# Performance work log

Measured on AMD Instinct MI355X. Metric: run time of the kernel, lower is better.

## Reference

```python
import jax, jax.numpy as jnp
import numpy as np

B, V, H_DIM, W_DIM = 4, 4, 256, 384
D_SH = 1  # sh_degree=0, pred_color=False -> (0+1)^2
SCALE_MIN, SCALE_MAX = 1e-05, 30.0
EPS = 1e-08


def _quat_to_mat(q):  # (...,4) wxyz unit quat -> (...,3,3)
    w, x, y, z = q[..., 0], q[..., 1], q[..., 2], q[..., 3]
    return jnp.stack([
        jnp.stack([1 - 2 * (y * y + z * z), 2 * (x * y - w * z), 2 * (x * z + w * y)], -1),
        jnp.stack([2 * (x * y + w * z), 1 - 2 * (x * x + z * z), 2 * (y * z - w * x)], -1),
        jnp.stack([2 * (x * z - w * y), 2 * (y * z + w * x), 1 - 2 * (x * x + y * y)], -1),
    ], -2)


def _mat_to_quat_wxyz(m):  # (...,3,3) rotation -> (...,4) wxyz
    m00, m01, m02 = m[..., 0, 0], m[..., 0, 1], m[..., 0, 2]
    m10, m11, m12 = m[..., 1, 0], m[..., 1, 1], m[..., 1, 2]
    m20, m21, m22 = m[..., 2, 0], m[..., 2, 1], m[..., 2, 2]
    q_abs = jnp.sqrt(jnp.maximum(0.0, jnp.stack([
        1.0 + m00 + m11 + m22, 1.0 + m00 - m11 - m22,
        1.0 - m00 + m11 - m22, 1.0 - m00 - m11 + m22], -1)))
    cand = jnp.stack([
        jnp.stack([q_abs[..., 0] ** 2, m21 - m12, m02 - m20, m10 - m01], -1),
        jnp.stack([m21 - m12, q_abs[..., 1] ** 2, m10 + m01, m02 + m20], -1),
        jnp.stack([m02 - m20, m10 + m01, q_abs[..., 2] ** 2, m12 + m21], -1),
        jnp.stack([m10 - m01, m20 + m02, m21 + m12, q_abs[..., 3] ** 2], -1),
    ], -2)
    cand = cand / (2.0 * jnp.maximum(q_abs[..., None], 0.1))
    idx = jnp.argmax(q_abs, axis=-1)
    q = jnp.take_along_axis(cand, idx[..., None, None], axis=-2)[..., 0, :]
    return q / jnp.linalg.norm(q, axis=-1, keepdims=True)


def _quat_mul_wxyz(a, b):
    aw, ax, ay, az = a[..., 0], a[..., 1], a[..., 2], a[..., 3]
    bw, bx, by, bz = b[..., 0], b[..., 1], b[..., 2], b[..., 3]
    return jnp.stack([
        aw * bw - ax * bx - ay * by - az * bz,
        aw * bx + ax * bw + ay * bz - az * by,
        aw * by - ax * bz + ay * bw + az * bx,
        aw * bz + ax * by - ay * bx + az * bw], -1)


def setup_inputs() -> dict:
    key = jax.random.key(0)
    k1, k2, k3, k4, k5, k6 = jax.random.split(key, 6)
    # valid world->cam extrinsics: rotation from random unit quats + translation
    q = jax.random.normal(k1, (B, V, 4), jnp.float32)
    q = q / jnp.linalg.norm(q, axis=-1, keepdims=True)
    R = _quat_to_mat(q)
    t = jax.random.normal(k2, (B, V, 3), jnp.float32)
    ext = jnp.zeros((B, V, 4, 4), jnp.float32)
    ext = ext.at[..., :3, :3].set(R).at[..., :3, 3].set(t).at[..., 3, 3].set(1.0)
    # pixel-unit intrinsics
    f = W_DIM * (0.8 + 0.4 * jax.random.uniform(k3, (B, V), jnp.float32))
    intr = jnp.zeros((B, V, 3, 3), jnp.float32)
    intr = (intr.at[..., 0, 0].set(f).at[..., 1, 1].set(f)
                .at[..., 0, 2].set(W_DIM / 2).at[..., 1, 2].set(H_DIM / 2)
                .at[..., 2, 2].set(1.0))
    depths = 0.5 + 9.5 * jax.random.uniform(k4, (B, V, H_DIM, W_DIM), jnp.float32)
    opac = jax.random.uniform(k5, (B, V, H_DIM, W_DIM), jnp.float32)
    raw = jax.random.normal(k6, (B, V, H_DIM, W_DIM, 12), jnp.float32)
    return {"extrinsics": ext, "intrinsics": intr, "depths": depths,
            "opacities": opac, "raw_gaussians": raw, "H": H_DIM, "W": W_DIM}


def reference(extrinsics, intrinsics, depths, opacities, raw_gaussians, H, W):
    raw = raw_gaussians
    b, v = raw.shape[:2]
    dtype = raw.dtype
    # cam2world = affine inverse of world2cam extrinsics
    Rw2c = extrinsics[..., :3, :3]
    t = extrinsics[..., :3, 3]
    Rc2w = jnp.swapaxes(Rw2c, -1, -2)                       # (b,v,3,3)
    origins = -jnp.einsum('bvij,bvj->bvi', Rc2w, t)          # (b,v,3) camera centers
    # normalized intrinsics (detached in the original)
    intr_n = jax.lax.stop_gradient(intrinsics) * jnp.array(
        [[1.0 / W], [1.0 / H], [1.0]], dtype=intrinsics.dtype)
    # pixel-center grid in normalized [0,1] coords, (x, y) order
    xs = (jnp.arange(W, dtype=dtype) + 0.5) / W
    ys = (jnp.arange(H, dtype=dtype) + 0.5) / H
    xy = jnp.stack(jnp.meshgrid(xs, ys, indexing='xy'), -1)  # (H,W,2)
    pixel_size = jnp.array([1.0 / W, 1.0 / H], dtype=dtype)
    xy = xy[None, None] + raw[..., :2] * pixel_size          # (b,v,H,W,2) with xy offset
    # unproject: K^-1 @ [x,y,1], normalize, rotate into world
    Kinv = jnp.linalg.inv(intr_n)                            # (b,v,3,3)
    homog = jnp.concatenate([xy, jnp.ones_like(xy[..., :1])], -1)
    d_cam = jnp.einsum('bvij,bvhwj->bvhwi', Kinv, homog)
    d_cam = d_cam / jnp.linalg.norm(d_cam, axis=-1, keepdims=True)
    d_world = jnp.einsum('bvij,bvhwj->bvhwi', Rc2w, d_cam)
    means = origins[:, :, None, None] + d_world * depths[..., None]
    means = means.reshape(b, -1, 3)
    # scales: sigmoid squash then metric scaling by depth * intrinsics multiplier
    scales = SCALE_MIN + (SCALE_MAX - SCALE_MIN) * jax.nn.sigmoid(raw[..., 2:5])
    k2 = intr_n[..., :2, :2]
    det = k2[..., 0, 0] * k2[..., 1, 1] - k2[..., 0, 1] * k2[..., 1, 0]
    inv2 = jnp.stack([
        jnp.stack([k2[..., 1, 1], -k2[..., 0, 1]], -1),
        jnp.stack([-k2[..., 1, 0], k2[..., 0, 0]], -1)], -2) / det[..., None, None]
    mult = 0.1 * jnp.einsum('bvij,j->bvi', inv2, pixel_size).sum(-1)  # (b,v)
    gs_scales = (scales * depths[..., None] * mult[:, :, None, None, None]).reshape(b, -1, 3)
    # rotations: normalize predicted cam quat (xyzw), compose with c2w rotation -> world wxyz
    rot = raw[..., 5:9]
    rot = rot / (jnp.linalg.norm(rot, axis=-1, keepdims=True) + EPS)
    cam_q_wxyz = jnp.concatenate([rot[..., 3:4], rot[..., :3]], -1)
    c2w_q = _mat_to_quat_wxyz(Rc2w)                          # (b,v,4)
    world_q = _quat_mul_wxyz(c2w_q[:, :, None, None, :], cam_q_wxyz)
    rotations = world_q.reshape(b, -1, 4)
    # spherical harmonics: degree 0 -> sh_mask is all ones, no SH rotation
    harmonics = raw[..., 9:12].reshape(b, -1, 3, D_SH)
    opac = opacities.reshape(b, -1)
    return means, gs_scales, rotations, harmonics, opac
```

## Files before the change

kernel.cpp:

```cpp
#include <hip/hip_runtime.h>
#include <math.h>

#define Bc 4
#define Vc 4
#define Hc 256
#define Wc 384
#define HWc (Hc*Wc)
#define TOTc (Bc*Vc*HWc)
#define SCALE_MIN_c 1e-05f
#define SCALE_MAX_c 30.0f
#define EPS_c 1e-08f

#define MEANS_OFF  ((size_t)0)
#define SCALES_OFF ((size_t)TOTc*3)
#define ROT_OFF    ((size_t)TOTc*6)
#define HARM_OFF   ((size_t)TOTc*10)
#define OPAC_OFF   ((size_t)TOTc*13)

__device__ __forceinline__ void async_copy16(const float4* g, float4* l) {
    __builtin_amdgcn_global_load_lds(
        (const __attribute__((address_space(1))) void*)g,
        (__attribute__((address_space(3))) void*)l,
        16, 0, 0);
}

__global__ __launch_bounds__(256) void ga_kernel(
    const float* __restrict__ ext,
    const float* __restrict__ intr,
    const float* __restrict__ depths,
    const float* __restrict__ opac,
    const float* __restrict__ raw,
    float* __restrict__ out)
{
    __shared__ float4 sRaw[768];
    __shared__ float sR[9];
    __shared__ float sO[3];
    __shared__ float sK[9];
    __shared__ float sQ[4];
    __shared__ float sMult;
    __shared__ float sOut[2304];

    const int tid = threadIdx.x;
    const int g   = blockIdx.x * 256 + tid;

    {
        const float4* gbase = reinterpret_cast<const float4*>(raw) + (size_t)blockIdx.x * 768;
        const int waveBase = tid & 192;
        async_copy16(gbase +   0 + tid, &sRaw[  0 + waveBase]);
        async_copy16(gbase + 256 + tid, &sRaw[256 + waveBase]);
        async_copy16(gbase + 512 + tid, &sRaw[512 + waveBase]);
    }

    const float dep = depths[g];
    const float op  = opac[g];

    if (tid == 0) {
        const int view = blockIdx.x / (HWc / 256);
        const float* E = ext + view * 16;
        float R[9];
        #pragma unroll
        for (int i = 0; i < 3; i++)
            #pragma unroll
            for (int j = 0; j < 3; j++)
                R[i*3+j] = E[j*4+i];
        const float t0 = E[3], t1 = E[7], t2 = E[11];
        sO[0] = -(R[0]*t0 + R[1]*t1 + R[2]*t2);
        sO[1] = -(R[3]*t0 + R[4]*t1 + R[5]*t2);
        sO[2] = -(R[6]*t0 + R[7]*t1 + R[8]*t2);
        #pragma unroll
        for (int k = 0; k < 9; k++) sR[k] = R[k];

        const float* I = intr + view * 9;
        const float a00 = I[0]*(1.0f/Wc), a01 = I[1]*(1.0f/Wc), a02 = I[2]*(1.0f/Wc);
        const float a10 = I[3]*(1.0f/Hc), a11 = I[4]*(1.0f/Hc), a12 = I[5]*(1.0f/Hc);
        const float a20 = I[6],           a21 = I[7],           a22 = I[8];
        const float det = a00*(a11*a22 - a12*a21)
                        - a01*(a10*a22 - a12*a20)
                        + a02*(a10*a21 - a11*a20);
        const float id = 1.0f / det;
        sK[0] = (a11*a22 - a12*a21)*id;
        sK[1] = (a02*a21 - a01*a22)*id;
        sK[2] = (a01*a12 - a02*a11)*id;
        sK[3] = (a12*a20 - a10*a22)*id;
        sK[4] = (a00*a22 - a02*a20)*id;
        sK[5] = (a02*a10 - a00*a12)*id;
        sK[6] = (a10*a21 - a11*a20)*id;
        sK[7] = (a01*a20 - a00*a21)*id;
        sK[8] = (a00*a11 - a01*a10)*id;

        const float det2 = a00*a11 - a01*a10;
        const float psx = 1.0f/Wc, psy = 1.0f/Hc;
        sMult = 0.1f * ((a11*psx - a01*psy) + (-a10*psx + a00*psy)) / det2;

        const float m00 = R[0], m01 = R[1], m02 = R[2];
        const float m10 = R[3], m11 = R[4], m12 = R[5];
        const float m20 = R[6], m21 = R[7], m22 = R[8];
        float qa[4];
        qa[0] = sqrtf(fmaxf(0.0f, 1.0f + m00 + m11 + m22));
        qa[1] = sqrtf(fmaxf(0.0f, 1.0f + m00 - m11 - m22));
        qa[2] = sqrtf(fmaxf(0.0f, 1.0f - m00 + m11 - m22));
        qa[3] = sqrtf(fmaxf(0.0f, 1.0f - m00 - m11 + m22));
        float cand[4][4] = {
            { qa[0]*qa[0], m21 - m12,   m02 - m20,   m10 - m01 },
            { m21 - m12,   qa[1]*qa[1], m10 + m01,   m02 + m20 },
            { m02 - m20,   m10 + m01,   qa[2]*qa[2], m12 + m21 },
            { m10 - m01,   m20 + m02,   m21 + m12,   qa[3]*qa[3] } };
        int idx = 0;
        if (qa[1] > qa[idx]) idx = 1;
        if (qa[2] > qa[idx]) idx = 2;
        if (qa[3] > qa[idx]) idx = 3;
        const float dd = 1.0f / (2.0f * fmaxf(qa[idx], 0.1f));
        float q0 = cand[idx][0]*dd, q1 = cand[idx][1]*dd,
              q2 = cand[idx][2]*dd, q3 = cand[idx][3]*dd;
        const float qn = 1.0f / sqrtf(q0*q0 + q1*q1 + q2*q2 + q3*q3);
        sQ[0] = q0*qn; sQ[1] = q1*qn; sQ[2] = q2*qn; sQ[3] = q3*qn;
    }
    __syncthreads();

    const float4 r0 = sRaw[tid*3 + 0];
    const float4 r1 = sRaw[tid*3 + 1];
    const float4 r2 = sRaw[tid*3 + 2];

    const int pix = g % HWc;
    const int h = pix / Wc;
    const int w = pix % Wc;

    const float x = (w + 0.5f) * (1.0f/Wc) + r0.x * (1.0f/Wc);
    const float y = (h + 0.5f) * (1.0f/Hc) + r0.y * (1.0f/Hc);

    float dc0 = sK[0]*x + sK[1]*y + sK[2];
    float dc1 = sK[3]*x + sK[4]*y + sK[5];
    float dc2 = sK[6]*x + sK[7]*y + sK[8];
    const float inl = rsqrtf(dc0*dc0 + dc1*dc1 + dc2*dc2);
    dc0 *= inl; dc1 *= inl; dc2 *= inl;

    const float dw0 = sR[0]*dc0 + sR[1]*dc1 + sR[2]*dc2;
    const float dw1 = sR[3]*dc0 + sR[4]*dc1 + sR[5]*dc2;
    const float dw2 = sR[6]*dc0 + sR[7]*dc1 + sR[8]*dc2;

    sOut[tid*3 + 0] = sO[0] + dw0 * dep;
    sOut[tid*3 + 1] = sO[1] + dw1 * dep;
    sOut[tid*3 + 2] = sO[2] + dw2 * dep;

    const float sm = dep * sMult;
    sOut[768 + tid*3 + 0] = (SCALE_MIN_c + (SCALE_MAX_c - SCALE_MIN_c) / (1.0f + __expf(-r0.z))) * sm;
    sOut[768 + tid*3 + 1] = (SCALE_MIN_c + (SCALE_MAX_c - SCALE_MIN_c) / (1.0f + __expf(-r0.w))) * sm;
    sOut[768 + tid*3 + 2] = (SCALE_MIN_c + (SCALE_MAX_c - SCALE_MIN_c) / (1.0f + __expf(-r1.x))) * sm;

    const float rx = r1.y, ry = r1.z, rz = r1.w, rw = r2.x;
    const float rn = 1.0f / (sqrtf(rx*rx + ry*ry + rz*rz + rw*rw) + EPS_c);
    const float bw = rw*rn, bx = rx*rn, by = ry*rn, bz = rz*rn;
    const float aw = sQ[0], ax = sQ[1], ay = sQ[2], az = sQ[3];
    float4 wq;
    wq.x = aw*bw - ax*bx - ay*by - az*bz;
    wq.y = aw*bx + ax*bw + ay*bz - az*by;
    wq.z = aw*by - ax*bz + ay*bw + az*bx;
    wq.w = aw*bz + ax*by - ay*bx + az*bw;
    reinterpret_cast<float4*>(out + ROT_OFF)[g] = wq;

    sOut[1536 + tid*3 + 0] = r2.y;
    sOut[1536 + tid*3 + 1] = r2.z;
    sOut[1536 + tid*3 + 2] = r2.w;

    out[OPAC_OFF + g] = op;

    __syncthreads();

    const float4* sv = reinterpret_cast<const float4*>(sOut);
    #pragma unroll
    for (int i = tid; i < 576; i += 256) {
        const int sec = i / 192;
        const int j   = i - sec * 192;
        const size_t base = (sec == 0 ? MEANS_OFF : (sec == 1 ? SCALES_OFF : HARM_OFF))
                          + (size_t)blockIdx.x * 768;
        reinterpret_cast<float4*>(out + base)[j] = sv[i];
    }
}

extern "C" void kernel_launch(void* const* d_in, const int* in_sizes, int n_in,
                              void* d_out, int out_size, void* d_ws, size_t ws_size,
                              hipStream_t stream) {
    const float* ext    = (const float*)d_in[0];
    const float* intr   = (const float*)d_in[1];
    const float* depths = (const float*)d_in[2];
    const float* opac   = (const float*)d_in[3];
    const float* raw    = (const float*)d_in[4];
    float* out = (float*)d_out;

    ga_kernel<<<TOTc / 256, 256, 0, stream>>>(ext, intr, depths, opac, raw, out);
}
```

Measured before the change: 171.2 us.

## Compute per-view constants per thread and drop block barriers via per-wave LDS staging

Every thread now computes the per-view rotation, inverse intrinsics and camera quaternion redundantly instead of thread 0 writing them to shared memory. This removes the block-wide barrier and the separate output staging buffer. Each wave async-loads its own slice of raw data, waits with s_waitcnt, and reuses the same LDS slots to repack results. Output stores become per-lane scalar writes instead of float4 writes, and the launch bounds request higher occupancy. The trade is extra redundant ALU work and scalar loads per thread, plus narrower global stores, in exchange for fewer barriers and less LDS.

```diff
diff --git a/kernel.cpp b/kernel.cpp
--- a/kernel.cpp
+++ b/kernel.cpp
@@ -24,7 +24,7 @@
         16, 0, 0);
 }
 
-__global__ __launch_bounds__(256) void ga_kernel(
+__global__ __launch_bounds__(256, 6) void ga_kernel(
     const float* __restrict__ ext,
     const float* __restrict__ intr,
     const float* __restrict__ depths,
@@ -33,89 +33,92 @@
     float* __restrict__ out)
 {
     __shared__ float4 sRaw[768];
-    __shared__ float sR[9];
-    __shared__ float sO[3];
-    __shared__ float sK[9];
-    __shared__ float sQ[4];
-    __shared__ float sMult;
-    __shared__ float sOut[2304];
 
-    const int tid = threadIdx.x;
-    const int g   = blockIdx.x * 256 + tid;
+    const int tid  = threadIdx.x;
+    const int lane = tid & 63;
+    const int wv   = tid >> 6;
+    const int g    = blockIdx.x * 256 + tid;
 
     {
-        const float4* gbase = reinterpret_cast<const float4*>(raw) + (size_t)blockIdx.x * 768;
-        const int waveBase = tid & 192;
-        async_copy16(gbase +   0 + tid, &sRaw[  0 + waveBase]);
-        async_copy16(gbase + 256 + tid, &sRaw[256 + waveBase]);
-        async_copy16(gbase + 512 + tid, &sRaw[512 + waveBase]);
+        const float4* gbase = reinterpret_cast<const float4*>(raw)
+                            + (size_t)blockIdx.x * 768 + wv * 192;
+        float4* lbase = &sRaw[wv * 192];
+        async_copy16(gbase +   0 + lane, lbase +   0);
+        async_copy16(gbase +  64 + lane, lbase +  64);
+        async_copy16(gbase + 128 + lane, lbase + 128);
     }
 
     const float dep = depths[g];
     const float op  = opac[g];
 
-    if (tid == 0) {
-        const int view = blockIdx.x / (HWc / 256);
-        const float* E = ext + view * 16;
-        float R[9];
-        #pragma unroll
-        for (int i = 0; i < 3; i++)
-            #pragma unroll
-            for (int j = 0; j < 3; j++)
-                R[i*3+j] = E[j*4+i];
-        const float t0 = E[3], t1 = E[7], t2 = E[11];
-        sO[0] = -(R[0]*t0 + R[1]*t1 + R[2]*t2);
-        sO[1] = -(R[3]*t0 + R[4]*t1 + R[5]*t2);
-        sO[2] = -(R[6]*t0 + R[7]*t1 + R[8]*t2);
-        #pragma unroll
-        for (int k = 0; k < 9; k++) sR[k] = R[k];
+    const int view = blockIdx.x / (HWc / 256);
+    const float* E = ext  + view * 16;
+    const float* I = intr + view * 9;
 
-        const float* I = intr + view * 9;
-        const float a00 = I[0]*(1.0f/Wc), a01 = I[1]*(1.0f/Wc), a02 = I[2]*(1.0f/Wc);
-        const float a10 = I[3]*(1.0f/Hc), a11 = I[4]*(1.0f/Hc), a12 = I[5]*(1.0f/Hc);
-        const float a20 = I[6],           a21 = I[7],           a22 = I[8];
-        const float det = a00*(a11*a22 - a12*a21)
-                        - a01*(a10*a22 - a12*a20)
-                        + a02*(a10*a21 - a11*a20);
-        const float id = 1.0f / det;
-        sK[0] = (a11*a22 - a12*a21)*id;
-        sK[1] = (a02*a21 - a01*a22)*id;
-        sK[2] = (a01*a12 - a02*a11)*id;
-        sK[3] = (a12*a20 - a10*a22)*id;
-        sK[4] = (a00*a22 - a02*a20)*id;
-        sK[5] = (a02*a10 - a00*a12)*id;
-        sK[6] = (a10*a21 - a11*a20)*id;
-        sK[7] = (a01*a20 - a00*a21)*id;
-        sK[8] = (a00*a11 - a01*a10)*id;
+    const float R0 = E[0], R1 = E[4], R2 = E[8];
+    const float R3 = E[1], R4 = E[5], R5 = E[9];
+    const float R6 = E[2], R7 = E[6], R8 = E[10];
+    const float t0 = E[3], t1 = E[7], t2 = E[11];
+    const float O0 = -(R0*t0 + R1*t1 + R2*t2);
+    const float O1 = -(R3*t0 + R4*t1 + R5*t2);
+    const float O2 = -(R6*t0 + R7*t1 + R8*t2);
 
-        const float det2 = a00*a11 - a01*a10;
-        const float psx = 1.0f/Wc, psy = 1.0f/Hc;
-        sMult = 0.1f * ((a11*psx - a01*psy) + (-a10*psx + a00*psy)) / det2;
+    const float a00 = I[0]*(1.0f/Wc), a01 = I[1]*(1.0f/Wc), a02 = I[2]*(1.0f/Wc);
+    const float a10 = I[3]*(1.0f/Hc), a11 = I[4]*(1.0f/Hc), a12 = I[5]*(1.0f/Hc);
+    const float a20 = I[6],           a21 = I[7],           a22 = I[8];
+    const float det = a00*(a11*a22 - a12*a21)
+                    - a01*(a10*a22 - a12*a20)
+                    + a02*(a10*a21 - a11*a20);
+    const float id = 1.0f / det;
+    const float K0 = (a11*a22 - a12*a21)*id;
+    const float K1 = (a02*a21 - a01*a22)*id;
+    const float K2 = (a01*a12 - a02*a11)*id;
+    const float K3 = (a12*a20 - a10*a22)*id;
+    const float K4 = (a00*a22 - a02*a20)*id;
+    const float K5 = (a02*a10 - a00*a12)*id;
+    const float K6 = (a10*a21 - a11*a20)*id;
+    const float K7 = (a01*a20 - a00*a21)*id;
+    const float K8 = (a00*a11 - a01*a10)*id;
 
-        const float m00 = R[0], m01 = R[1], m02 = R[2];
-        const float m10 = R[3], m11 = R[4], m12 = R[5];
-        const float m20 = R[6], m21 = R[7], m22 = R[8];
-        float qa[4];
-        qa[0] = sqrtf(fmaxf(0.0f, 1.0f + m00 + m11 + m22));
-        qa[1] = sqrtf(fmaxf(0.0f, 1.0f + m00 - m11 - m22));
-        qa[2] = sqrtf(fmaxf(0.0f, 1.0f - m00 + m11 - m22));
-        qa[3] = sqrtf(fmaxf(0.0f, 1.0f - m00 - m11 + m22));
-        float cand[4][4] = {
-            { qa[0]*qa[0], m21 - m12,   m02 - m20,   m10 - m01 },
-            { m21 - m12,   qa[1]*qa[1], m10 + m01,   m02 + m20 },
-            { m02 - m20,   m10 + m01,   qa[2]*qa[2], m12 + m21 },
-            { m10 - m01,   m20 + m02,   m21 + m12,   qa[3]*qa[3] } };
-        int idx = 0;
-        if (qa[1] > qa[idx]) idx = 1;
-        if (qa[2] > qa[idx]) idx = 2;
-        if (qa[3] > qa[idx]) idx = 3;
-        const float dd = 1.0f / (2.0f * fmaxf(qa[idx], 0.1f));
-        float q0 = cand[idx][0]*dd, q1 = cand[idx][1]*dd,
-              q2 = cand[idx][2]*dd, q3 = cand[idx][3]*dd;
-        const float qn = 1.0f / sqrtf(q0*q0 + q1*q1 + q2*q2 + q3*q3);
-        sQ[0] = q0*qn; sQ[1] = q1*qn; sQ[2] = q2*qn; sQ[3] = q3*qn;
+    const float det2 = a00*a11 - a01*a10;
+    const float mult = 0.1f * ((a11*(1.0f/Wc) - a01*(1.0f/Hc))
+                             + (-a10*(1.0f/Wc) + a00*(1.0f/Hc))) / det2;
+
+    const float m00 = R0, m01 = R1, m02 = R2;
+    const float m10 = R3, m11 = R4, m12 = R5;
+    const float m20 = R6, m21 = R7, m22 = R8;
+    const float qa0 = sqrtf(fmaxf(0.0f, 1.0f + m00 + m11 + m22));
+    const float qa1 = sqrtf(fmaxf(0.0f, 1.0f + m00 - m11 - m22));
+    const float qa2 = sqrtf(fmaxf(0.0f, 1.0f - m00 + m11 - m22));
+    const float qa3 = sqrtf(fmaxf(0.0f, 1.0f - m00 - m11 + m22));
+    float bq = qa0;
+    float b0 = qa0*qa0, b1 = m21 - m12, b2 = m02 - m20, b3 = m10 - m01;
+    {
+        const bool s1 = qa1 > bq;
+        b0 = s1 ? (m21 - m12) : b0;
+        b1 = s1 ? (qa1*qa1)   : b1;
+        b2 = s1 ? (m10 + m01) : b2;
+        b3 = s1 ? (m02 + m20) : b3;
+        bq = s1 ? qa1 : bq;
+        const bool s2 = qa2 > bq;
+        b0 = s2 ? (m02 - m20) : b0;
+        b1 = s2 ? (m10 + m01) : b1;
+        b2 = s2 ? (qa2*qa2)   : b2;
+        b3 = s2 ? (m12 + m21) : b3;
+        bq = s2 ? qa2 : bq;
+        const bool s3 = qa3 > bq;
+        b0 = s3 ? (m10 - m01) : b0;
+        b1 = s3 ? (m20 + m02) : b1;
+        b2 = s3 ? (m21 + m12) : b2;
+        b3 = s3 ? (qa3*qa3)   : b3;
+        bq = s3 ? qa3 : bq;
     }
-    __syncthreads();
+    const float dd = 1.0f / (2.0f * fmaxf(bq, 0.1f));
+    const float q0 = b0*dd, q1 = b1*dd, q2 = b2*dd, q3 = b3*dd;
+    const float qn = 1.0f / sqrtf(q0*q0 + q1*q1 + q2*q2 + q3*q3);
+    const float aw = q0*qn, ax = q1*qn, ay = q2*qn, az = q3*qn;
+
+    asm volatile("s_waitcnt vmcnt(0)" ::: "memory");
 
     const float4 r0 = sRaw[tid*3 + 0];
     const float4 r1 = sRaw[tid*3 + 1];
@@ -123,57 +126,58 @@
 
     const int pix = g % HWc;
     const int h = pix / Wc;
-    const int w = pix % Wc;
+    const int w = pix - h * Wc;
 
     const float x = (w + 0.5f) * (1.0f/Wc) + r0.x * (1.0f/Wc);
     const float y = (h + 0.5f) * (1.0f/Hc) + r0.y * (1.0f/Hc);
 
-    float dc0 = sK[0]*x + sK[1]*y + sK[2];
-    float dc1 = sK[3]*x + sK[4]*y + sK[5];
-    float dc2 = sK[6]*x + sK[7]*y + sK[8];
+    float dc0 = K0*x + K1*y + K2;
+    float dc1 = K3*x + K4*y + K5;
+    float dc2 = K6*x + K7*y + K8;
     const float inl = rsqrtf(dc0*dc0 + dc1*dc1 + dc2*dc2);
     dc0 *= inl; dc1 *= inl; dc2 *= inl;
 
-    const float dw0 = sR[0]*dc0 + sR[1]*dc1 + sR[2]*dc2;
-    const float dw1 = sR[3]*dc0 + sR[4]*dc1 + sR[5]*dc2;
-    const float dw2 = sR[6]*dc0 + sR[7]*dc1 + sR[8]*dc2;
+    const float dw0 = R0*dc0 + R1*dc1 + R2*dc2;
+    const float dw1 = R3*dc0 + R4*dc1 + R5*dc2;
+    const float dw2 = R6*dc0 + R7*dc1 + R8*dc2;
 
-    sOut[tid*3 + 0] = sO[0] + dw0 * dep;
-    sOut[tid*3 + 1] = sO[1] + dw1 * dep;
-    sOut[tid*3 + 2] = sO[2] + dw2 * dep;
-
-    const float sm = dep * sMult;
-    sOut[768 + tid*3 + 0] = (SCALE_MIN_c + (SCALE_MAX_c - SCALE_MIN_c) / (1.0f + __expf(-r0.z))) * sm;
-    sOut[768 + tid*3 + 1] = (SCALE_MIN_c + (SCALE_MAX_c - SCALE_MIN_c) / (1.0f + __expf(-r0.w))) * sm;
-    sOut[768 + tid*3 + 2] = (SCALE_MIN_c + (SCALE_MAX_c - SCALE_MIN_c) / (1.0f + __expf(-r1.x))) * sm;
+    const float sm  = dep * mult;
+    const float sc0 = (SCALE_MIN_c + (SCALE_MAX_c - SCALE_MIN_c) / (1.0f + __expf(-r0.z))) * sm;
+    const float sc1 = (SCALE_MIN_c + (SCALE_MAX_c - SCALE_MIN_c) / (1.0f + __expf(-r0.w))) * sm;
+    const float sc2 = (SCALE_MIN_c + (SCALE_MAX_c - SCALE_MIN_c) / (1.0f + __expf(-r1.x))) * sm;
 
     const float rx = r1.y, ry = r1.z, rz = r1.w, rw = r2.x;
     const float rn = 1.0f / (sqrtf(rx*rx + ry*ry + rz*rz + rw*rw) + EPS_c);
-    const float bw = rw*rn, bx = rx*rn, by = ry*rn, bz = rz*rn;
-    const float aw = sQ[0], ax = sQ[1], ay = sQ[2], az = sQ[3];
+    const float bwq = rw*rn, bxq = rx*rn, byq = ry*rn, bzq = rz*rn;
     float4 wq;
-    wq.x = aw*bw - ax*bx - ay*by - az*bz;
-    wq.y = aw*bx + ax*bw + ay*bz - az*by;
-    wq.z = aw*by - ax*bz + ay*bw + az*bx;
-    wq.w = aw*bz + ax*by - ay*bx + az*bw;
+    wq.x = aw*bwq - ax*bxq - ay*byq - az*bzq;
+    wq.y = aw*bxq + ax*bwq + ay*bzq - az*byq;
+    wq.z = aw*byq - ax*bzq + ay*bwq + az*bxq;
+    wq.w = aw*bzq + ax*byq - ay*bxq + az*bwq;
     reinterpret_cast<float4*>(out + ROT_OFF)[g] = wq;
-
-    sOut[1536 + tid*3 + 0] = r2.y;
-    sOut[1536 + tid*3 + 1] = r2.z;
-    sOut[1536 + tid*3 + 2] = r2.w;
 
     out[OPAC_OFF + g] = op;
 
-    __syncthreads();
+    float4 A, Bv;
+    A.x = O0 + dw0*dep;  A.y = O1 + dw1*dep;  A.z = O2 + dw2*dep;  A.w = sc0;
+    Bv.x = sc1;  Bv.y = sc2;  Bv.z = r2.y;  Bv.w = r2.z;
+    sRaw[tid*3 + 0] = A;
+    sRaw[tid*3 + 1] = Bv;
+    reinterpret_cast<float*>(sRaw)[tid*12 + 8] = r2.w;
 
-    const float4* sv = reinterpret_cast<const float4*>(sOut);
+    const float* sF = reinterpret_cast<const float*>(sRaw);
+    float* outM = out + MEANS_OFF  + (size_t)blockIdx.x * 768;
+    float* outS = out + SCALES_OFF + (size_t)blockIdx.x * 768;
+    float* outH = out + HARM_OFF   + (size_t)blockIdx.x * 768;
     #pragma unroll
-    for (int i = tid; i < 576; i += 256) {
-        const int sec = i / 192;
-        const int j   = i - sec * 192;
-        const size_t base = (sec == 0 ? MEANS_OFF : (sec == 1 ? SCALES_OFF : HARM_OFF))
-                          + (size_t)blockIdx.x * 768;
-        reinterpret_cast<float4*>(out + base)[j] = sv[i];
+    for (int k = 0; k < 3; ++k) {
+        const int off  = wv*192 + k*64 + lane;
+        const int p    = off / 3;
+        const int c    = off - p*3;
+        const int base = p*12 + c;
+        outM[off] = sF[base + 0];
+        outS[off] = sF[base + 3];
+        outH[off] = sF[base + 6];
     }
 }
 
```

Result: no change. 170.6 us (-0.4%).
